# Optimization experiments

Hardware: AMD Instinct MI355X
Metric: run time of the kernel (lower is better)

## Reference

```python
import jax, jax.numpy as jnp
import numpy as np

B, T, IN, H, OUT = 256, 100, 128, 1024, 35
BITS = 4
SLOPE = 25.0
THR_H = 1.0
THR_O = 1.0
BETA1, BETA2, BETA3, BETA4 = 0.9, 0.85, 0.8, 0.95


def fake_quant(w, w_min, w_max, bits=BITS):
    # FakeQuantize in training mode: STE -> forward value is quantized, grad passes through clamp
    levels = 2 ** bits
    scale = (w_max - w_min) / (levels - 1)
    wc = jnp.clip(w, w_min, w_max)
    q = jnp.round((wc - w_min) / scale) * scale + w_min
    return wc + jax.lax.stop_gradient(q - wc)


@jax.custom_vjp
def spike(x):
    # Heaviside forward, fast-sigmoid surrogate backward (snn.surrogate.fast_sigmoid)
    return (x > 0).astype(x.dtype)

def _spike_fwd(x):
    return (x > 0).astype(x.dtype), x

def _spike_bwd(x, g):
    return (g / (SLOPE * jnp.abs(x) + 1.0) ** 2,)

spike.defvjp(_spike_fwd, _spike_bwd)


def lif_step(cur, mem, beta, thr, reset_mechanism):
    # snntorch Leaky (reset_delay semantics): reset computed from previous mem, detached
    reset = jax.lax.stop_gradient((mem > thr).astype(cur.dtype))
    base = beta * mem + cur
    if reset_mechanism == "subtract":
        mem_new = base - reset * thr
    else:  # "zero"
        mem_new = base - reset * base
    spk = spike(mem_new - thr)
    return spk, mem_new


def setup_inputs() -> dict:
    key = jax.random.key(0)
    ks = jax.random.split(key, 5)
    x = jax.random.normal(ks[0], (B, T, IN), dtype=jnp.float32)
    # QuantLinear init: uniform(w_min, w_max); fc1 uses (-0.5, 0.5), others (0.001, 1.0)
    w1 = jax.random.uniform(ks[1], (H, IN), minval=-0.5, maxval=0.5, dtype=jnp.float32)
    w2 = jax.random.uniform(ks[2], (H, H), minval=0.001, maxval=1.0, dtype=jnp.float32)
    w3 = jax.random.uniform(ks[3], (H, H), minval=0.001, maxval=1.0, dtype=jnp.float32)
    w4 = jax.random.uniform(ks[4], (OUT, H), minval=0.001, maxval=1.0, dtype=jnp.float32)
    return {"x": x, "w1": w1, "w2": w2, "w3": w3, "w4": w4}


def reference(x, w1, w2, w3, w4):
    # hoist weight quantization out of the time loop (identical math each step)
    q1 = fake_quant(w1, -0.5, 0.5)
    q2 = fake_quant(w2, 0.001, 1.0)
    q3 = fake_quant(w3, 0.001, 1.0)
    q4 = fake_quant(w4, 0.001, 1.0)
    xs = jnp.transpose(x, (1, 0, 2)) / 15.0  # [T, B, IN]
    Bx = x.shape[0]

    def step(carry, xt):
        m1, m2, m3, m4 = carry
        s1, m1 = lif_step(xt @ q1.T, m1, BETA1, THR_H, "subtract")
        s2, m2 = lif_step(s1 @ q2.T, m2, BETA2, THR_H, "subtract")
        s3, m3 = lif_step(s2 @ q3.T, m3, BETA3, THR_H, "subtract")
        s4, m4 = lif_step(s3 @ q4.T, m4, BETA4, THR_O, "zero")
        return (m1, m2, m3, m4), (s1, s2, s3, s4, m4)

    init = (jnp.zeros((Bx, H), x.dtype), jnp.zeros((Bx, H), x.dtype),
            jnp.zeros((Bx, H), x.dtype), jnp.zeros((Bx, OUT), x.dtype))
    _, (spk1, spk2, spk3, spk4, mem4) = jax.lax.scan(step, init, xs)
    # stacked along time dim 0, matching torch.stack(dim=0)
    return spk1, spk2, spk3, spk4, mem4
```

## Files before the change

kernel.cpp:

```cpp
#include <hip/hip_runtime.h>
#include <stdint.h>

#define NB  256
#define NT  100
#define NIN 128
#define NH  1024
#define NOUT 35

#define O_SPK2 26214400ull
#define O_SPK3 52428800ull
#define O_SPK4 78643200ull
#define O_MEM4 79539200ull

#define WS_XT   0ull
#define WS_Q1T  13107200ull
#define WS_K2T  13631488ull
#define WS_K3T  14680064ull
#define WS_K4T  15728640ull

#define S2C ((float)((1.0 - 0.001) / 15.0))
#define S1C ((float)(1.0 / 15.0))

__global__ void k_prep(const float* __restrict__ x, const float* __restrict__ w1,
                       const float* __restrict__ w2, const float* __restrict__ w3,
                       const float* __restrict__ w4, uint8_t* __restrict__ ws)
{
  long long id = (long long)blockIdx.x * 256 + threadIdx.x;
  if (id < 1048576) {
    int i = (int)(id >> 10), j = (int)(id & 1023);
    float wv = w2[(size_t)j * 1024 + i];
    float wc = fminf(fmaxf(wv, 0.001f), 1.0f);
    ws[WS_K2T + id] = (uint8_t)(int)rintf((wc - 0.001f) / S2C);
    return;
  }
  id -= 1048576;
  if (id < 1048576) {
    int i = (int)(id >> 10), j = (int)(id & 1023);
    float wv = w3[(size_t)j * 1024 + i];
    float wc = fminf(fmaxf(wv, 0.001f), 1.0f);
    ws[WS_K3T + id] = (uint8_t)(int)rintf((wc - 0.001f) / S2C);
    return;
  }
  id -= 1048576;
  if (id < 49152) {
    int i = (int)(id / 48), j = (int)(id % 48);
    uint8_t v = 0;
    if (j < NOUT) {
      float wv = w4[(size_t)j * 1024 + i];
      float wc = fminf(fmaxf(wv, 0.001f), 1.0f);
      v = (uint8_t)(int)rintf((wc - 0.001f) / S2C);
    }
    ws[WS_K4T + id] = v;
    return;
  }
  id -= 49152;
  if (id < 131072) {
    int i = (int)(id >> 10), j = (int)(id & 1023);
    float wv = w1[(size_t)j * 128 + i];
    float wc = fminf(fmaxf(wv, -0.5f), 0.5f);
    float q = rintf((wc + 0.5f) / S1C) * S1C - 0.5f;
    ((float*)(ws + WS_Q1T))[id] = q;
    return;
  }
  id -= 131072;
  if (id < 3276800) {
    int row = (int)(id >> 7), i = (int)(id & 127);
    int tt = row >> 8, bb = row & 255;
    ((float*)(ws + WS_XT))[id] = x[((size_t)bb * NT + tt) * NIN + i] / 15.0f;
  }
}

__global__ __launch_bounds__(512, 1) void k_spk1(const float* __restrict__ xt,
                                                 const float* __restrict__ q1T,
                                                 float* __restrict__ out)
{
  __shared__ float xs[25 * 128];
  const int b = blockIdx.x;
  const int tid = threadIdx.x;
  float m1a = 0.f, m1b = 0.f;

  for (int c = 0; c < 4; ++c) {
    __syncthreads();
    {
      int e = tid;
      int tt = e >> 5, iq = e & 31;
      ((float4*)xs)[e] = *(const float4*)(xt + ((size_t)(c * 25 + tt) * NB + b) * NIN + iq * 4);
      e = tid + 512;
      if (e < 800) {
        tt = e >> 5; iq = e & 31;
        ((float4*)xs)[e] = *(const float4*)(xt + ((size_t)(c * 25 + tt) * NB + b) * NIN + iq * 4);
      }
    }
    __syncthreads();

    float acc0[25], acc1[25];
    #pragma unroll
    for (int tt = 0; tt < 25; ++tt) { acc0[tt] = 0.f; acc1[tt] = 0.f; }

    for (int ib = 0; ib < 16; ++ib) {
      float q0[8], q1v[8];
      #pragma unroll
      for (int u = 0; u < 8; ++u) {
        q0[u]  = q1T[(size_t)(ib * 8 + u) * NH + tid];
        q1v[u] = q1T[(size_t)(ib * 8 + u) * NH + tid + 512];
      }
      #pragma unroll
      for (int tt = 0; tt < 25; ++tt) {
        const float4 xa = *(const float4*)&xs[tt * 128 + ib * 8];
        const float4 xb = *(const float4*)&xs[tt * 128 + ib * 8 + 4];
        acc0[tt] = fmaf(xa.x, q0[0], acc0[tt]);
        acc0[tt] = fmaf(xa.y, q0[1], acc0[tt]);
        acc0[tt] = fmaf(xa.z, q0[2], acc0[tt]);
        acc0[tt] = fmaf(xa.w, q0[3], acc0[tt]);
        acc0[tt] = fmaf(xb.x, q0[4], acc0[tt]);
        acc0[tt] = fmaf(xb.y, q0[5], acc0[tt]);
        acc0[tt] = fmaf(xb.z, q0[6], acc0[tt]);
        acc0[tt] = fmaf(xb.w, q0[7], acc0[tt]);
        acc1[tt] = fmaf(xa.x, q1v[0], acc1[tt]);
        acc1[tt] = fmaf(xa.y, q1v[1], acc1[tt]);
        acc1[tt] = fmaf(xa.z, q1v[2], acc1[tt]);
        acc1[tt] = fmaf(xa.w, q1v[3], acc1[tt]);
        acc1[tt] = fmaf(xb.x, q1v[4], acc1[tt]);
        acc1[tt] = fmaf(xb.y, q1v[5], acc1[tt]);
        acc1[tt] = fmaf(xb.z, q1v[6], acc1[tt]);
        acc1[tt] = fmaf(xb.w, q1v[7], acc1[tt]);
      }
    }
    #pragma unroll
    for (int tt = 0; tt < 25; ++tt) {
      const int t = c * 25 + tt;
      const size_t row = ((size_t)t * NB + b) * (size_t)NH;
      float rst0 = m1a > 1.0f ? 1.0f : 0.0f;
      m1a = fmaf(0.9f, m1a, acc0[tt]) - rst0;
      out[row + tid] = ((m1a - 1.0f) > 0.0f) ? 1.0f : 0.0f;
      float rst1 = m1b > 1.0f ? 1.0f : 0.0f;
      m1b = fmaf(0.9f, m1b, acc1[tt]) - rst1;
      out[row + tid + 512] = ((m1b - 1.0f) > 0.0f) ? 1.0f : 0.0f;
    }
  }
}

#define ACC(V) do { \
  aE0 += (V).x & 0x00FF00FFu; aO0 += ((V).x >> 8) & 0x00FF00FFu; \
  aE1 += (V).y & 0x00FF00FFu; aO1 += ((V).y >> 8) & 0x00FF00FFu; \
  aE2 += (V).z & 0x00FF00FFu; aO2 += ((V).z >> 8) & 0x00FF00FFu; \
  aE3 += (V).w & 0x00FF00FFu; aO3 += ((V).w >> 8) & 0x00FF00FFu; } while (0)

__global__ __launch_bounds__(512, 1) void k_main(
    const uint8_t* __restrict__ k2T, const uint8_t* __restrict__ k3T,
    const uint8_t* __restrict__ k4T, float* __restrict__ out)
{
  const int b = blockIdx.x;
  const int tid = threadIdx.x;
  const int lane = tid & 63;
  const int wave = tid >> 6;

  __shared__ uint16_t list[1024];
  __shared__ uint4    pEa4[512];
  __shared__ uint4    pOa4[512];
  __shared__ uint4    wcnt4[2];
  uint32_t* pEa  = (uint32_t*)pEa4;
  uint32_t* pOa  = (uint32_t*)pOa4;
  uint32_t* wcnt = (uint32_t*)wcnt4;

  float m2[2] = {0.f, 0.f}, m3[2] = {0.f, 0.f}, m4 = 0.f;
  uint32_t nT, nL; bool cm;

  auto buildList = [&](uint64_t bA, uint64_t bB) {
    const uint4 c0 = wcnt4[0], c1 = wcnt4[1];
    nT = c0.x + c0.y + c0.z + c0.w + c1.x + c1.y + c1.z + c1.w;
    cm = nT > 512;
    nL = cm ? (1024u - nT) : nT;
    uint32_t pre = 0;
    pre += (wave > 0) ? c0.x : 0u;  pre += (wave > 1) ? c0.y : 0u;
    pre += (wave > 2) ? c0.z : 0u;  pre += (wave > 3) ? c0.w : 0u;
    pre += (wave > 4) ? c1.x : 0u;  pre += (wave > 5) ? c1.y : 0u;
    pre += (wave > 6) ? c1.z : 0u;
    const uint32_t bs = cm ? ((uint32_t)(wave << 7) - pre) : pre;
    const uint64_t cA = cm ? ~bA : bA;
    const uint64_t cB = cm ? ~bB : bB;
    const uint64_t ltm = (1ull << lane) - 1ull;
    if ((cA >> lane) & 1ull)
      list[bs + (uint32_t)__popcll(cA & ltm)] = (uint16_t)tid;
    if ((cB >> lane) & 1ull)
      list[bs + (uint32_t)__popcll(cA) + (uint32_t)__popcll(cB & ltm)] = (uint16_t)(tid + 512);
  };

  auto gatherBig = [&](const uint8_t* __restrict__ mat, uint32_t nLv) {
    uint32_t aE0=0,aE1=0,aE2=0,aE3=0,aO0=0,aO1=0,aO2=0,aO3=0;
    const uint8_t* bp = mat + (lane << 4);
    uint32_t a = (uint32_t)wave;
    for (; a + 24 < nLv; a += 32) {
      uint32_t i0 = (uint32_t)__builtin_amdgcn_readfirstlane((int)list[a]);
      uint32_t i1 = (uint32_t)__builtin_amdgcn_readfirstlane((int)list[a + 8]);
      uint32_t i2 = (uint32_t)__builtin_amdgcn_readfirstlane((int)list[a + 16]);
      uint32_t i3 = (uint32_t)__builtin_amdgcn_readfirstlane((int)list[a + 24]);
      const uint4 v0 = *(const uint4*)(bp + ((size_t)i0 << 10));
      const uint4 v1 = *(const uint4*)(bp + ((size_t)i1 << 10));
      const uint4 v2 = *(const uint4*)(bp + ((size_t)i2 << 10));
      const uint4 v3 = *(const uint4*)(bp + ((size_t)i3 << 10));
      ACC(v0); ACC(v1); ACC(v2); ACC(v3);
    }
    for (; a < nLv; a += 8) {
      uint32_t i0 = (uint32_t)__builtin_amdgcn_readfirstlane((int)list[a]);
      const uint4 v0 = *(const uint4*)(bp + ((size_t)i0 << 10));
      ACC(v0);
    }
    const int basei = (wave << 8) + (lane << 2);
    *(uint4*)&pEa[basei] = make_uint4(aE0, aE1, aE2, aE3);
    *(uint4*)&pOa[basei] = make_uint4(aO0, aO1, aO2, aO3);
  };

  auto gatherAll = [&](const uint8_t* __restrict__ mat) {
    uint32_t aE0=0,aE1=0,aE2=0,aE3=0,aO0=0,aO1=0,aO2=0,aO3=0;
    const uint8_t* bp = mat + (lane << 4);
    for (uint32_t a = (uint32_t)wave; a + 24 < 1024u; a += 32) {
      const uint4 v0 = *(const uint4*)(bp + ((size_t)a << 10));
      const uint4 v1 = *(const uint4*)(bp + ((size_t)(a + 8) << 10));
      const uint4 v2 = *(const uint4*)(bp + ((size_t)(a + 16) << 10));
      const uint4 v3 = *(const uint4*)(bp + ((size_t)(a + 24) << 10));
      ACC(v0); ACC(v1); ACC(v2); ACC(v3);
    }
    const int basei = (wave << 8) + (lane << 2);
    *(uint4*)&pEa[basei] = make_uint4(aE0, aE1, aE2, aE3);
    *(uint4*)&pOa[basei] = make_uint4(aO0, aO1, aO2, aO3);
  };

  auto gather4 = [&](uint32_t nLv) {
    uint32_t aE0=0,aE1=0,aE2=0,aE3=0,aO0=0,aO1=0,aO2=0,aO3=0;
    const uint8_t* bp = k4T + (lane << 4);
    uint32_t a = (uint32_t)wave;
    for (; a + 24 < nLv; a += 32) {
      uint32_t i0 = (uint32_t)__builtin_amdgcn_readfirstlane((int)list[a]);
      uint32_t i1 = (uint32_t)__builtin_amdgcn_readfirstlane((int)list[a + 8]);
      uint32_t i2 = (uint32_t)__builtin_amdgcn_readfirstlane((int)list[a + 16]);
      uint32_t i3 = (uint32_t)__builtin_amdgcn_readfirstlane((int)list[a + 24]);
      const uint4 v0 = *(const uint4*)(bp + (size_t)i0 * 48u);
      const uint4 v1 = *(const uint4*)(bp + (size_t)i1 * 48u);
      const uint4 v2 = *(const uint4*)(bp + (size_t)i2 * 48u);
      const uint4 v3 = *(const uint4*)(bp + (size_t)i3 * 48u);
      ACC(v0); ACC(v1); ACC(v2); ACC(v3);
    }
    for (; a < nLv; a += 8) {
      uint32_t i0 = (uint32_t)__builtin_amdgcn_readfirstlane((int)list[a]);
      const uint4 v0 = *(const uint4*)(bp + (size_t)i0 * 48u);
      ACC(v0);
    }
    const int basei = (wave << 8) + (lane << 2);
    *(uint4*)&pEa[basei] = make_uint4(aE0, aE1, aE2, aE3);
    *(uint4*)&pOa[basei] = make_uint4(aO0, aO1, aO2, aO3);
  };

  auto gather4All = [&]() {
    uint32_t aE0=0,aE1=0,aE2=0,aE3=0,aO0=0,aO1=0,aO2=0,aO3=0;
    const uint8_t* bp = k4T + (lane << 4);
    for (uint32_t a = (uint32_t)wave; a + 24 < 1024u; a += 32) {
      const uint4 v0 = *(const uint4*)(bp + (size_t)a * 48u);
      const uint4 v1 = *(const uint4*)(bp + (size_t)(a + 8) * 48u);
      const uint4 v2 = *(const uint4*)(bp + (size_t)(a + 16) * 48u);
      const uint4 v3 = *(const uint4*)(bp + (size_t)(a + 24) * 48u);
      ACC(v0); ACC(v1); ACC(v2); ACC(v3);
    }
    const int basei = (wave << 8) + (lane << 2);
    *(uint4*)&pEa[basei] = make_uint4(aE0, aE1, aE2, aE3);
    *(uint4*)&pOa[basei] = make_uint4(aO0, aO1, aO2, aO3);
  };

  auto gsum = [&](int jn) -> uint32_t {
    const int w = jn >> 2, sh = (jn & 2) << 3;
    const uint32_t* P = (jn & 1) ? pOa : pEa;
    uint32_t s = 0;
    #pragma unroll
    for (int g = 0; g < 8; ++g) s += P[(g << 8) + w];
    return (s >> sh) & 0xffffu;
  };

  gatherAll(k2T);
  __syncthreads();
  uint32_t r2[2]; r2[0] = gsum(tid); r2[1] = gsum(tid + 512);
  __syncthreads();
  gatherAll(k3T);
  __syncthreads();
  uint32_t r3[2]; r3[0] = gsum(tid); r3[1] = gsum(tid + 512);
  __syncthreads();
  if (lane < 3) gather4All();
  __syncthreads();
  const uint32_t r4v = (tid < NOUT) ? gsum(tid) : 0u;

  float s1a = out[(size_t)b * NH + tid];
  float s1b = out[(size_t)b * NH + tid + 512];

  for (int t = 0; t < NT; ++t) {
    const size_t rowH = ((size_t)t * NB + b) * (size_t)NH;
    const size_t rowO = ((size_t)t * NB + b) * (size_t)NOUT;

    bool sA = s1a > 0.5f, sB = s1b > 0.5f;
    {
      int tn = (t + 1 < NT) ? (t + 1) : t;
      size_t rowN = ((size_t)tn * NB + b) * (size_t)NH;
      s1a = out[rowN + tid];
      s1b = out[rowN + tid + 512];
    }
    uint64_t bA = __ballot(sA), bB = __ballot(sB);
    if (lane == 0) wcnt[wave] = (uint32_t)(__popcll(bA) + __popcll(bB));
    __syncthreads();
    buildList(bA, bB);
    __syncthreads();
    const uint32_t n1 = nT, nl1 = nL; const bool cm1 = cm;
    if (nl1) gatherBig(k2T, nl1);
    __syncthreads();

    {
      float nb = 0.001f * (float)n1;
      #pragma unroll
      for (int c = 0; c < 2; ++c) {
        int j = (c << 9) + tid;
        uint32_t gsv = nl1 ? gsum(j) : 0u;
        uint32_t K = cm1 ? (r2[c] - gsv) : gsv;
        float cur = fmaf(S2C, (float)K, nb);
        float rst = m2[c] > 1.0f ? 1.0f : 0.0f;
        m2[c] = fmaf(0.85f, m2[c], cur) - rst;
        bool sp = (m2[c] - 1.0f) > 0.0f;
        out[O_SPK2 + rowH + j] = sp ? 1.0f : 0.0f;
        if (c == 0) sA = sp; else sB = sp;
      }
    }
    bA = __ballot(sA); bB = __ballot(sB);
    if (lane == 0) wcnt[wave] = (uint32_t)(__popcll(bA) + __popcll(bB));
    __syncthreads();
    buildList(bA, bB);
    __syncthreads();
    const uint32_t n2 = nT, nl2 = nL; const bool cm2 = cm;
    if (nl2) gatherBig(k3T, nl2);
    __syncthreads();

    {
      float nb = 0.001f * (float)n2;
      #pragma unroll
      for (int c = 0; c < 2; ++c) {
        int j = (c << 9) + tid;
        uint32_t gsv = nl2 ? gsum(j) : 0u;
        uint32_t K = cm2 ? (r3[c] - gsv) : gsv;
        float cur = fmaf(S2C, (float)K, nb);
        float rst = m3[c] > 1.0f ? 1.0f : 0.0f;
        m3[c] = fmaf(0.8f, m3[c], cur) - rst;
        bool sp = (m3[c] - 1.0f) > 0.0f;
        out[O_SPK3 + rowH + j] = sp ? 1.0f : 0.0f;
        if (c == 0) sA = sp; else sB = sp;
      }
    }
    bA = __ballot(sA); bB = __ballot(sB);
    if (lane == 0) wcnt[wave] = (uint32_t)(__popcll(bA) + __popcll(bB));
    __syncthreads();
    buildList(bA, bB);
    __syncthreads();
    const uint32_t n3 = nT, nl3 = nL; const bool cm3 = cm;

    if (nl3 && lane < 3) gather4(nl3);
    __syncthreads();

    if (tid < NOUT) {
      uint32_t gsv = nl3 ? gsum(tid) : 0u;
      uint32_t K = cm3 ? (r4v - gsv) : gsv;
      float cur = fmaf(S2C, (float)K, 0.001f * (float)n3);
      float rst = m4 > 1.0f ? 1.0f : 0.0f;
      float bsv = fmaf(0.95f, m4, cur);
      m4 = (rst > 0.0f) ? 0.0f : bsv;
      out[O_SPK4 + rowO + tid] = ((m4 - 1.0f) > 0.0f) ? 1.0f : 0.0f;
      out[O_MEM4 + rowO + tid] = m4;
    }
  }
}
#undef ACC

extern "C" void kernel_launch(void* const* d_in, const int* in_sizes, int n_in,
                              void* d_out, int out_size, void* d_ws, size_t ws_size,
                              hipStream_t stream)
{
  const float* x  = (const float*)d_in[0];
  const float* w1 = (const float*)d_in[1];
  const float* w2 = (const float*)d_in[2];
  const float* w3 = (const float*)d_in[3];
  const float* w4 = (const float*)d_in[4];
  float* out = (float*)d_out;
  uint8_t* ws = (uint8_t*)d_ws;
  hipLaunchKernelGGL(k_prep, dim3(21696), dim3(256), 0, stream, x, w1, w2, w3, w4, ws);
  hipLaunchKernelGGL(k_spk1, dim3(256),   dim3(512), 0, stream,
                     (const float*)(ws + WS_XT), (const float*)(ws + WS_Q1T), out);
  hipLaunchKernelGGL(k_main, dim3(256),   dim3(512), 0, stream,
                     ws + WS_K2T, ws + WS_K3T, ws + WS_K4T, out);
}
```

Baseline: 693.2 us.

## Pack quantized weights into 4-bit nibbles and retile spk1 to 256 threads

Quantized weight codes for layers 2-4 are now stored two per byte, which halves the bytes each spike-driven row gather reads. The SWAR accumulators are rewritten for 4-bit fields in 16-bit lanes, and gsum's index mapping is changed to match. Separately, the layer-1 kernel now uses 256 threads with four output columns each, so every shared x value is reused across more accumulators. The risks are more shift/mask ALU work per gathered byte, higher register pressure in spk1 (100 accumulators), and fewer threads per block there.

Measured after the change: 772.9 us. +11.5%, slower.

```diff
diff --git a/kernel.cpp b/kernel.cpp
--- a/kernel.cpp
+++ b/kernel.cpp
@@ -21,39 +21,41 @@
 #define S2C ((float)((1.0 - 0.001) / 15.0))
 #define S1C ((float)(1.0 / 15.0))
 
+__device__ __forceinline__ uint32_t kq(float wv) {
+  float wc = fminf(fmaxf(wv, 0.001f), 1.0f);
+  return (uint32_t)(int)rintf((wc - 0.001f) / S2C);
+}
+
 __global__ void k_prep(const float* __restrict__ x, const float* __restrict__ w1,
                        const float* __restrict__ w2, const float* __restrict__ w3,
                        const float* __restrict__ w4, uint8_t* __restrict__ ws)
 {
   long long id = (long long)blockIdx.x * 256 + threadIdx.x;
-  if (id < 1048576) {
-    int i = (int)(id >> 10), j = (int)(id & 1023);
-    float wv = w2[(size_t)j * 1024 + i];
-    float wc = fminf(fmaxf(wv, 0.001f), 1.0f);
-    ws[WS_K2T + id] = (uint8_t)(int)rintf((wc - 0.001f) / S2C);
+  if (id < 524288) {
+    int i = (int)(id >> 9), jp = (int)(id & 511);
+    uint32_t ka = kq(w2[(size_t)(2 * jp) * 1024 + i]);
+    uint32_t kb = kq(w2[(size_t)(2 * jp + 1) * 1024 + i]);
+    ws[WS_K2T + id] = (uint8_t)(ka | (kb << 4));
     return;
   }
-  id -= 1048576;
-  if (id < 1048576) {
-    int i = (int)(id >> 10), j = (int)(id & 1023);
-    float wv = w3[(size_t)j * 1024 + i];
-    float wc = fminf(fmaxf(wv, 0.001f), 1.0f);
-    ws[WS_K3T + id] = (uint8_t)(int)rintf((wc - 0.001f) / S2C);
+  id -= 524288;
+  if (id < 524288) {
+    int i = (int)(id >> 9), jp = (int)(id & 511);
+    uint32_t ka = kq(w3[(size_t)(2 * jp) * 1024 + i]);
+    uint32_t kb = kq(w3[(size_t)(2 * jp + 1) * 1024 + i]);
+    ws[WS_K3T + id] = (uint8_t)(ka | (kb << 4));
     return;
   }
-  id -= 1048576;
-  if (id < 49152) {
-    int i = (int)(id / 48), j = (int)(id % 48);
-    uint8_t v = 0;
-    if (j < NOUT) {
-      float wv = w4[(size_t)j * 1024 + i];
-      float wc = fminf(fmaxf(wv, 0.001f), 1.0f);
-      v = (uint8_t)(int)rintf((wc - 0.001f) / S2C);
-    }
-    ws[WS_K4T + id] = v;
+  id -= 524288;
+  if (id < 24576) {
+    int i = (int)(id / 24), bp = (int)(id % 24);
+    int j0 = 2 * bp, j1 = 2 * bp + 1;
+    uint32_t ka = (j0 < NOUT) ? kq(w4[(size_t)j0 * 1024 + i]) : 0u;
+    uint32_t kb = (j1 < NOUT) ? kq(w4[(size_t)j1 * 1024 + i]) : 0u;
+    ws[WS_K4T + id] = (uint8_t)(ka | (kb << 4));
     return;
   }
-  id -= 49152;
+  id -= 24576;
   if (id < 131072) {
     int i = (int)(id >> 10), j = (int)(id & 1023);
     float wv = w1[(size_t)j * 128 + i];
@@ -70,85 +72,79 @@
   }
 }
 
-__global__ __launch_bounds__(512, 1) void k_spk1(const float* __restrict__ xt,
+__global__ __launch_bounds__(256, 1) void k_spk1(const float* __restrict__ xt,
                                                  const float* __restrict__ q1T,
                                                  float* __restrict__ out)
 {
   __shared__ float xs[25 * 128];
   const int b = blockIdx.x;
   const int tid = threadIdx.x;
-  float m1a = 0.f, m1b = 0.f;
+  float m[4] = {0.f, 0.f, 0.f, 0.f};
 
   for (int c = 0; c < 4; ++c) {
     __syncthreads();
-    {
-      int e = tid;
-      int tt = e >> 5, iq = e & 31;
-      ((float4*)xs)[e] = *(const float4*)(xt + ((size_t)(c * 25 + tt) * NB + b) * NIN + iq * 4);
-      e = tid + 512;
+    #pragma unroll
+    for (int k = 0; k < 4; ++k) {
+      int e = tid + k * 256;
       if (e < 800) {
-        tt = e >> 5; iq = e & 31;
+        int tt = e >> 5, iq = e & 31;
         ((float4*)xs)[e] = *(const float4*)(xt + ((size_t)(c * 25 + tt) * NB + b) * NIN + iq * 4);
       }
     }
     __syncthreads();
 
-    float acc0[25], acc1[25];
+    float acc[4][25];
     #pragma unroll
-    for (int tt = 0; tt < 25; ++tt) { acc0[tt] = 0.f; acc1[tt] = 0.f; }
-
+    for (int tt = 0; tt < 25; ++tt) {
+      acc[0][tt] = 0.f; acc[1][tt] = 0.f; acc[2][tt] = 0.f; acc[3][tt] = 0.f;
+    }
     for (int ib = 0; ib < 16; ++ib) {
-      float q0[8], q1v[8];
+      float q0[8], q1v[8], q2v[8], q3v[8];
       #pragma unroll
       for (int u = 0; u < 8; ++u) {
-        q0[u]  = q1T[(size_t)(ib * 8 + u) * NH + tid];
-        q1v[u] = q1T[(size_t)(ib * 8 + u) * NH + tid + 512];
+        const float* qp = q1T + (size_t)(ib * 8 + u) * NH + tid;
+        q0[u]  = qp[0];
+        q1v[u] = qp[256];
+        q2v[u] = qp[512];
+        q3v[u] = qp[768];
       }
       #pragma unroll
       for (int tt = 0; tt < 25; ++tt) {
         const float4 xa = *(const float4*)&xs[tt * 128 + ib * 8];
         const float4 xb = *(const float4*)&xs[tt * 128 + ib * 8 + 4];
-        acc0[tt] = fmaf(xa.x, q0[0], acc0[tt]);
-        acc0[tt] = fmaf(xa.y, q0[1], acc0[tt]);
-        acc0[tt] = fmaf(xa.z, q0[2], acc0[tt]);
-        acc0[tt] = fmaf(xa.w, q0[3], acc0[tt]);
-        acc0[tt] = fmaf(xb.x, q0[4], acc0[tt]);
-        acc0[tt] = fmaf(xb.y, q0[5], acc0[tt]);
-        acc0[tt] = fmaf(xb.z, q0[6], acc0[tt]);
-        acc0[tt] = fmaf(xb.w, q0[7], acc0[tt]);
-        acc1[tt] = fmaf(xa.x, q1v[0], acc1[tt]);
-        acc1[tt] = fmaf(xa.y, q1v[1], acc1[tt]);
-        acc1[tt] = fmaf(xa.z, q1v[2], acc1[tt]);
-        acc1[tt] = fmaf(xa.w, q1v[3], acc1[tt]);
-        acc1[tt] = fmaf(xb.x, q1v[4], acc1[tt]);
-        acc1[tt] = fmaf(xb.y, q1v[5], acc1[tt]);
-        acc1[tt] = fmaf(xb.z, q1v[6], acc1[tt]);
-        acc1[tt] = fmaf(xb.w, q1v[7], acc1[tt]);
+        float xr[8] = {xa.x, xa.y, xa.z, xa.w, xb.x, xb.y, xb.z, xb.w};
+        #pragma unroll
+        for (int u = 0; u < 8; ++u) {
+          acc[0][tt] = fmaf(xr[u], q0[u],  acc[0][tt]);
+          acc[1][tt] = fmaf(xr[u], q1v[u], acc[1][tt]);
+          acc[2][tt] = fmaf(xr[u], q2v[u], acc[2][tt]);
+          acc[3][tt] = fmaf(xr[u], q3v[u], acc[3][tt]);
+        }
       }
     }
     #pragma unroll
     for (int tt = 0; tt < 25; ++tt) {
       const int t = c * 25 + tt;
       const size_t row = ((size_t)t * NB + b) * (size_t)NH;
-      float rst0 = m1a > 1.0f ? 1.0f : 0.0f;
-      m1a = fmaf(0.9f, m1a, acc0[tt]) - rst0;
-      out[row + tid] = ((m1a - 1.0f) > 0.0f) ? 1.0f : 0.0f;
-      float rst1 = m1b > 1.0f ? 1.0f : 0.0f;
-      m1b = fmaf(0.9f, m1b, acc1[tt]) - rst1;
-      out[row + tid + 512] = ((m1b - 1.0f) > 0.0f) ? 1.0f : 0.0f;
-    }
-  }
-}
-
-#define ACC(V) do { \
-  aE0 += (V).x & 0x00FF00FFu; aO0 += ((V).x >> 8) & 0x00FF00FFu; \
-  aE1 += (V).y & 0x00FF00FFu; aO1 += ((V).y >> 8) & 0x00FF00FFu; \
-  aE2 += (V).z & 0x00FF00FFu; aO2 += ((V).z >> 8) & 0x00FF00FFu; \
-  aE3 += (V).w & 0x00FF00FFu; aO3 += ((V).w >> 8) & 0x00FF00FFu; } while (0)
+      #pragma unroll
+      for (int n = 0; n < 4; ++n) {
+        float rst = m[n] > 1.0f ? 1.0f : 0.0f;
+        m[n] = fmaf(0.9f, m[n], acc[n][tt]) - rst;
+        out[row + n * 256 + tid] = ((m[n] - 1.0f) > 0.0f) ? 1.0f : 0.0f;
+      }
+    }
+  }
+}
+
+#define ACCN(V) do { \
+  a00 += (V).x & 0x000F000Fu; a01 += ((V).x >> 4) & 0x000F000Fu; \
+  a02 += ((V).x >> 8) & 0x000F000Fu; a03 += ((V).x >> 12) & 0x000F000Fu; \
+  a10 += (V).y & 0x000F000Fu; a11 += ((V).y >> 4) & 0x000F000Fu; \
+  a12 += ((V).y >> 8) & 0x000F000Fu; a13 += ((V).y >> 12) & 0x000F000Fu; } while (0)
 
 __global__ __launch_bounds__(512, 1) void k_main(
-    const uint8_t* __restrict__ k2T, const uint8_t* __restrict__ k3T,
-    const uint8_t* __restrict__ k4T, float* __restrict__ out)
+    const uint8_t* __restrict__ k2P, const uint8_t* __restrict__ k3P,
+    const uint8_t* __restrict__ k4P, float* __restrict__ out)
 {
   const int b = blockIdx.x;
   const int tid = threadIdx.x;
@@ -187,99 +183,100 @@
   };
 
   auto gatherBig = [&](const uint8_t* __restrict__ mat, uint32_t nLv) {
-    uint32_t aE0=0,aE1=0,aE2=0,aE3=0,aO0=0,aO1=0,aO2=0,aO3=0;
-    const uint8_t* bp = mat + (lane << 4);
+    uint32_t a00=0,a01=0,a02=0,a03=0,a10=0,a11=0,a12=0,a13=0;
+    const uint8_t* bp = mat + (lane << 3);
     uint32_t a = (uint32_t)wave;
     for (; a + 24 < nLv; a += 32) {
       uint32_t i0 = (uint32_t)__builtin_amdgcn_readfirstlane((int)list[a]);
       uint32_t i1 = (uint32_t)__builtin_amdgcn_readfirstlane((int)list[a + 8]);
       uint32_t i2 = (uint32_t)__builtin_amdgcn_readfirstlane((int)list[a + 16]);
       uint32_t i3 = (uint32_t)__builtin_amdgcn_readfirstlane((int)list[a + 24]);
-      const uint4 v0 = *(const uint4*)(bp + ((size_t)i0 << 10));
-      const uint4 v1 = *(const uint4*)(bp + ((size_t)i1 << 10));
-      const uint4 v2 = *(const uint4*)(bp + ((size_t)i2 << 10));
-      const uint4 v3 = *(const uint4*)(bp + ((size_t)i3 << 10));
-      ACC(v0); ACC(v1); ACC(v2); ACC(v3);
+      const uint2 v0 = *(const uint2*)(bp + ((size_t)i0 << 9));
+      const uint2 v1 = *(const uint2*)(bp + ((size_t)i1 << 9));
+      const uint2 v2 = *(const uint2*)(bp + ((size_t)i2 << 9));
+      const uint2 v3 = *(const uint2*)(bp + ((size_t)i3 << 9));
+      ACCN(v0); ACCN(v1); ACCN(v2); ACCN(v3);
     }
     for (; a < nLv; a += 8) {
       uint32_t i0 = (uint32_t)__builtin_amdgcn_readfirstlane((int)list[a]);
-      const uint4 v0 = *(const uint4*)(bp + ((size_t)i0 << 10));
-      ACC(v0);
+      const uint2 v0 = *(const uint2*)(bp + ((size_t)i0 << 9));
+      ACCN(v0);
     }
     const int basei = (wave << 8) + (lane << 2);
-    *(uint4*)&pEa[basei] = make_uint4(aE0, aE1, aE2, aE3);
-    *(uint4*)&pOa[basei] = make_uint4(aO0, aO1, aO2, aO3);
+    *(uint4*)&pEa[basei] = make_uint4(a00, a01, a02, a03);
+    *(uint4*)&pOa[basei] = make_uint4(a10, a11, a12, a13);
   };
 
   auto gatherAll = [&](const uint8_t* __restrict__ mat) {
-    uint32_t aE0=0,aE1=0,aE2=0,aE3=0,aO0=0,aO1=0,aO2=0,aO3=0;
-    const uint8_t* bp = mat + (lane << 4);
+    uint32_t a00=0,a01=0,a02=0,a03=0,a10=0,a11=0,a12=0,a13=0;
+    const uint8_t* bp = mat + (lane << 3);
     for (uint32_t a = (uint32_t)wave; a + 24 < 1024u; a += 32) {
-      const uint4 v0 = *(const uint4*)(bp + ((size_t)a << 10));
-      const uint4 v1 = *(const uint4*)(bp + ((size_t)(a + 8) << 10));
-      const uint4 v2 = *(const uint4*)(bp + ((size_t)(a + 16) << 10));
-      const uint4 v3 = *(const uint4*)(bp + ((size_t)(a + 24) << 10));
-      ACC(v0); ACC(v1); ACC(v2); ACC(v3);
+      const uint2 v0 = *(const uint2*)(bp + ((size_t)a << 9));
+      const uint2 v1 = *(const uint2*)(bp + ((size_t)(a + 8) << 9));
+      const uint2 v2 = *(const uint2*)(bp + ((size_t)(a + 16) << 9));
+      const uint2 v3 = *(const uint2*)(bp + ((size_t)(a + 24) << 9));
+      ACCN(v0); ACCN(v1); ACCN(v2); ACCN(v3);
     }
     const int basei = (wave << 8) + (lane << 2);
-    *(uint4*)&pEa[basei] = make_uint4(aE0, aE1, aE2, aE3);
-    *(uint4*)&pOa[basei] = make_uint4(aO0, aO1, aO2, aO3);
+    *(uint4*)&pEa[basei] = make_uint4(a00, a01, a02, a03);
+    *(uint4*)&pOa[basei] = make_uint4(a10, a11, a12, a13);
   };
 
   auto gather4 = [&](uint32_t nLv) {
-    uint32_t aE0=0,aE1=0,aE2=0,aE3=0,aO0=0,aO1=0,aO2=0,aO3=0;
-    const uint8_t* bp = k4T + (lane << 4);
+    uint32_t a00=0,a01=0,a02=0,a03=0,a10=0,a11=0,a12=0,a13=0;
+    const uint8_t* bp = k4P + (lane << 3);
     uint32_t a = (uint32_t)wave;
     for (; a + 24 < nLv; a += 32) {
       uint32_t i0 = (uint32_t)__builtin_amdgcn_readfirstlane((int)list[a]);
       uint32_t i1 = (uint32_t)__builtin_amdgcn_readfirstlane((int)list[a + 8]);
       uint32_t i2 = (uint32_t)__builtin_amdgcn_readfirstlane((int)list[a + 16]);
       uint32_t i3 = (uint32_t)__builtin_amdgcn_readfirstlane((int)list[a + 24]);
-      const uint4 v0 = *(const uint4*)(bp + (size_t)i0 * 48u);
-      const uint4 v1 = *(const uint4*)(bp + (size_t)i1 * 48u);
-      const uint4 v2 = *(const uint4*)(bp + (size_t)i2 * 48u);
-      const uint4 v3 = *(const uint4*)(bp + (size_t)i3 * 48u);
-      ACC(v0); ACC(v1); ACC(v2); ACC(v3);
+      const uint2 v0 = *(const uint2*)(bp + (size_t)i0 * 24u);
+      const uint2 v1 = *(const uint2*)(bp + (size_t)i1 * 24u);
+      const uint2 v2 = *(const uint2*)(bp + (size_t)i2 * 24u);
+      const uint2 v3 = *(const uint2*)(bp + (size_t)i3 * 24u);
+      ACCN(v0); ACCN(v1); ACCN(v2); ACCN(v3);
     }
     for (; a < nLv; a += 8) {
       uint32_t i0 = (uint32_t)__builtin_amdgcn_readfirstlane((int)list[a]);
-      const uint4 v0 = *(const uint4*)(bp + (size_t)i0 * 48u);
-      ACC(v0);
+      const uint2 v0 = *(const uint2*)(bp + (size_t)i0 * 24u);
+      ACCN(v0);
     }
     const int basei = (wave << 8) + (lane << 2);
-    *(uint4*)&pEa[basei] = make_uint4(aE0, aE1, aE2, aE3);
-    *(uint4*)&pOa[basei] = make_uint4(aO0, aO1, aO2, aO3);
+    *(uint4*)&pEa[basei] = make_uint4(a00, a01, a02, a03);
+    *(uint4*)&pOa[basei] = make_uint4(a10, a11, a12, a13);
   };
 
   auto gather4All = [&]() {
-    uint32_t aE0=0,aE1=0,aE2=0,aE3=0,aO0=0,aO1=0,aO2=0,aO3=0;
-    const uint8_t* bp = k4T + (lane << 4);
+    uint32_t a00=0,a01=0,a02=0,a03=0,a10=0,a11=0,a12=0,a13=0;
+    const uint8_t* bp = k4P + (lane << 3);
     for (uint32_t a = (uint32_t)wave; a + 24 < 1024u; a += 32) {
-      const uint4 v0 = *(const uint4*)(bp + (size_t)a * 48u);
-      const uint4 v1 = *(const uint4*)(bp + (size_t)(a + 8) * 48u);
-      const uint4 v2 = *(const uint4*)(bp + (size_t)(a + 16) * 48u);
-      const uint4 v3 = *(const uint4*)(bp + (size_t)(a + 24) * 48u);
-      ACC(v0); ACC(v1); ACC(v2); ACC(v3);
+      const uint2 v0 = *(const uint2*)(bp + (size_t)a * 24u);
+      const uint2 v1 = *(const uint2*)(bp + (size_t)(a + 8) * 24u);
+      const uint2 v2 = *(const uint2*)(bp + (size_t)(a + 16) * 24u);
+      const uint2 v3 = *(const uint2*)(bp + (size_t)(a + 24) * 24u);
+      ACCN(v0); ACCN(v1); ACCN(v2); ACCN(v3);
     }
     const int basei = (wave << 8) + (lane << 2);
-    *(uint4*)&pEa[basei] = make_uint4(aE0, aE1, aE2, aE3);
-    *(uint4*)&pOa[basei] = make_uint4(aO0, aO1, aO2, aO3);
+    *(uint4*)&pEa[basei] = make_uint4(a00, a01, a02, a03);
+    *(uint4*)&pOa[basei] = make_uint4(a10, a11, a12, a13);
   };
 
   auto gsum = [&](int jn) -> uint32_t {
-    const int w = jn >> 2, sh = (jn & 2) << 3;
-    const uint32_t* P = (jn & 1) ? pOa : pEa;
+    const int idx = ((jn >> 4) << 2) + (jn & 3);
+    const int sh = ((jn >> 2) & 1) << 4;
+    const uint32_t* P = ((jn >> 3) & 1) ? pOa : pEa;
     uint32_t s = 0;
     #pragma unroll
-    for (int g = 0; g < 8; ++g) s += P[(g << 8) + w];
+    for (int g = 0; g < 8; ++g) s += P[(g << 8) + idx];
     return (s >> sh) & 0xffffu;
   };
 
-  gatherAll(k2T);
+  gatherAll(k2P);
   __syncthreads();
   uint32_t r2[2]; r2[0] = gsum(tid); r2[1] = gsum(tid + 512);
   __syncthreads();
-  gatherAll(k3T);
+  gatherAll(k3P);
   __syncthreads();
   uint32_t r3[2]; r3[0] = gsum(tid); r3[1] = gsum(tid + 512);
   __syncthreads();
@@ -307,7 +304,7 @@
     buildList(bA, bB);
     __syncthreads();
     const uint32_t n1 = nT, nl1 = nL; const bool cm1 = cm;
-    if (nl1) gatherBig(k2T, nl1);
+    if (nl1) gatherBig(k2P, nl1);
     __syncthreads();
 
     {
@@ -331,7 +328,7 @@
     buildList(bA, bB);
     __syncthreads();
     const uint32_t n2 = nT, nl2 = nL; const bool cm2 = cm;
-    if (nl2) gatherBig(k3T, nl2);
+    if (nl2) gatherBig(k3P, nl2);
     __syncthreads();
 
     {
@@ -371,7 +368,7 @@
     }
   }
 }
-#undef ACC
+#undef ACCN
 
 extern "C" void kernel_launch(void* const* d_in, const int* in_sizes, int n_in,
                               void* d_out, int out_size, void* d_ws, size_t ws_size,
@@ -384,8 +381,8 @@
   const float* w4 = (const float*)d_in[4];
   float* out = (float*)d_out;
   uint8_t* ws = (uint8_t*)d_ws;
-  hipLaunchKernelGGL(k_prep, dim3(21696), dim3(256), 0, stream, x, w1, w2, w3, w4, ws);
-  hipLaunchKernelGGL(k_spk1, dim3(256),   dim3(512), 0, stream,
+  hipLaunchKernelGGL(k_prep, dim3(17504), dim3(256), 0, stream, x, w1, w2, w3, w4, ws);
+  hipLaunchKernelGGL(k_spk1, dim3(256),   dim3(256), 0, stream,
                      (const float*)(ws + WS_XT), (const float*)(ws + WS_Q1T), out);
   hipLaunchKernelGGL(k_main, dim3(256),   dim3(512), 0, stream,
                      ws + WS_K2T, ws + WS_K3T, ws + WS_K4T, out);
```
